# Optimization experiments

Measured on AMD Instinct MI355X. Metric: run time of the kernel, lower is better.

## Reference

```python
import jax, jax.numpy as jnp
import numpy as np

B, F, T, EPT, S, E, H, LVL = 16384, 512, 4, 2, 2, 256, 128, 2

def _ple_level(xs_task, x_sh, w_task, b_task, w_sh, b_sh, w_gate, b_gate, w_gsh=None, b_gsh=None):
    # xs_task: [T,B,I] per-task inputs; x_sh: [B,I] shared input
    task_out = jax.nn.relu(jnp.einsum('tbi,teio->tbeo', xs_task, w_task) + b_task[:, None])  # [T,B,EPT,E]
    sh_out = jax.nn.relu(jnp.einsum('bi,sio->bso', x_sh, w_sh) + b_sh)                       # [B,S,E]
    t = task_out.shape[0]
    experts = jnp.concatenate([task_out, jnp.broadcast_to(sh_out[None], (t,) + sh_out.shape)], axis=2)  # [T,B,EPT+S,E]
    gate = jax.nn.softmax(jnp.einsum('tbi,tig->tbg', xs_task, w_gate) + b_gate[:, None], axis=-1)
    task_next = jnp.einsum('tbg,tbge->tbe', gate, experts)  # [T,B,E]
    sh_next = None
    if w_gsh is not None:
        # all experts ordered task0_exp0, task0_exp1, task1_exp0, ..., then shared
        bsz = x_sh.shape[0]
        all_exp = jnp.concatenate([jnp.transpose(task_out, (1, 0, 2, 3)).reshape(bsz, -1, task_out.shape[-1]), sh_out], axis=1)
        gsh = jax.nn.softmax(x_sh @ w_gsh + b_gsh, axis=-1)
        sh_next = jnp.einsum('bg,bge->be', gsh, all_exp)
    return task_next, sh_next

def setup_inputs() -> dict:
    key = jax.random.key(0)
    ks = jax.random.split(key, 16)
    sc = 0.02
    d = {
        'x': jax.random.normal(ks[0], (B, F), jnp.float32),
        # level 0 (in_dim=F, has shared gate)
        'w_task0': jax.random.normal(ks[1], (T, EPT, F, E), jnp.float32) * sc,
        'b_task0': jnp.zeros((T, EPT, E), jnp.float32),
        'w_sh0': jax.random.normal(ks[2], (S, F, E), jnp.float32) * sc,
        'b_sh0': jnp.zeros((S, E), jnp.float32),
        'w_gate0': jax.random.normal(ks[3], (T, F, EPT + S), jnp.float32) * sc,
        'b_gate0': jnp.zeros((T, EPT + S), jnp.float32),
        'w_gsh0': jax.random.normal(ks[4], (F, T * EPT + S), jnp.float32) * sc,
        'b_gsh0': jnp.zeros((T * EPT + S,), jnp.float32),
        # level 1 (last; in_dim=E, no shared gate)
        'w_task1': jax.random.normal(ks[5], (T, EPT, E, E), jnp.float32) * sc,
        'b_task1': jnp.zeros((T, EPT, E), jnp.float32),
        'w_sh1': jax.random.normal(ks[6], (S, E, E), jnp.float32) * sc,
        'b_sh1': jnp.zeros((S, E), jnp.float32),
        'w_gate1': jax.random.normal(ks[7], (T, E, EPT + S), jnp.float32) * sc,
        'b_gate1': jnp.zeros((T, EPT + S), jnp.float32),
        # towers
        'w_tw': jax.random.normal(ks[8], (T, E, H), jnp.float32) * sc,
        'b_tw': jnp.zeros((T, H), jnp.float32),
        'w_out': jax.random.normal(ks[9], (T, H, 2), jnp.float32) * sc,
        'b_out': jnp.zeros((T, 2), jnp.float32),
    }
    return d

def reference(x, w_task0, b_task0, w_sh0, b_sh0, w_gate0, b_gate0, w_gsh0, b_gsh0,
              w_task1, b_task1, w_sh1, b_sh1, w_gate1, b_gate1,
              w_tw, b_tw, w_out, b_out):
    xs_task = jnp.broadcast_to(x[None], (T,) + x.shape)  # all tasks see same input at level 0
    t1, sh1 = _ple_level(xs_task, x, w_task0, b_task0, w_sh0, b_sh0, w_gate0, b_gate0, w_gsh0, b_gsh0)
    t2, _ = _ple_level(t1, sh1, w_task1, b_task1, w_sh1, b_sh1, w_gate1, b_gate1)
    h = jax.nn.relu(jnp.einsum('tbe,teh->tbh', t2, w_tw) + b_tw[:, None])
    logits = jnp.einsum('tbh,tho->tbo', h, w_out) + b_out[:, None]
    p = jax.nn.softmax(logits, axis=-1)
    return jnp.clip(p, 1e-15, 1.0 - 1e-15)  # [T,B,2]
```

## Files before the change

### kernel.cpp

```cpp
#include <hip/hip_runtime.h>

typedef unsigned short u16;
typedef __bf16 bf16x8 __attribute__((ext_vector_type(8)));
typedef float f32x4 __attribute__((ext_vector_type(4)));
typedef u16 u16x8 __attribute__((ext_vector_type(8)));

#define B_ 16384

__device__ __forceinline__ u16 f2b(float f){
  unsigned u = __builtin_bit_cast(unsigned, f);
  u = (u + 0x7FFFu + ((u >> 16) & 1u)) >> 16;
  return (u16)u;
}
__device__ __forceinline__ float b2f(u16 v){
  return __builtin_bit_cast(float, ((unsigned)v) << 16);
}
__device__ __forceinline__ void ld8(const u16* __restrict__ p, float* f){
  u16x8 v = *(const u16x8*)p;
  #pragma unroll
  for (int j = 0; j < 8; ++j) f[j] = b2f(v[j]);
}
__device__ __forceinline__ void st8(u16* __restrict__ p, const float* f){
  u16x8 v;
  #pragma unroll
  for (int j = 0; j < 8; ++j) v[j] = f2b(f[j]);
  *(u16x8*)p = v;
}

__device__ __forceinline__ void gload16(const u16* g, u16* lds){
  __builtin_amdgcn_global_load_lds(
      (const __attribute__((address_space(1))) unsigned int*)g,
      (__attribute__((address_space(3))) unsigned int*)lds, 16, 0, 0);
}

__device__ __forceinline__ void core32(const u16* __restrict__ A,
                                       const u16* __restrict__ Wt,
                                       int K, int m0, int n0, int nt,
                                       u16* sm, f32x4 acc[4][4])
{
  const int tid = threadIdx.x, lane = tid & 63, wave = tid >> 6;
  const int wm = ((tid >> 7) & 3) * 64;
  const int wn = ((tid >> 6) & 1) * 64;

  #pragma unroll
  for (int m = 0; m < 4; ++m)
    #pragma unroll
    for (int n = 0; n < 4; ++n) acc[m][n] = (f32x4){0.f, 0.f, 0.f, 0.f};

  const int s_    = (lane & 7) ^ ((lane >> 3) & 7);
  const int srow2 = 2 * (lane >> 3) + (s_ >> 2);
  const int sk    = (s_ & 3) * 8;
  const u16* gsrc[3];
  int gdst[3];
  #pragma unroll
  for (int i = 0; i < 3; ++i) {
    int c = wave * 3 + i;
    if (c < 16) {
      gsrc[i] = A + (size_t)(m0 + c * 16 + srow2) * K + sk;
      gdst[i] = c * 512;
    } else {
      gsrc[i] = Wt + (size_t)(n0 + (c - 16) * 16 + srow2) * K + sk;
      gdst[i] = 8192 + (c - 16) * 512;
    }
  }

  int aoff[4], boff[4];
  #pragma unroll
  for (int m = 0; m < 4; ++m) {
    int r = wm + m * 16 + (lane & 15);
    int L = r >> 1;
    int phys = (((r & 1) << 2) + (lane >> 4)) ^ (L & 7);
    aoff[m] = L * 64 + phys * 8;
  }
  #pragma unroll
  for (int n = 0; n < 4; ++n) {
    int r = wn + n * 16 + (lane & 15);
    int L = r >> 1;
    int phys = (((r & 1) << 2) + (lane >> 4)) ^ (L & 7);
    boff[n] = 8192 + L * 64 + phys * 8;
  }

  #pragma unroll
  for (int j = 0; j < 2; ++j) {
    u16* sl = sm + j * 12288;
    #pragma unroll
    for (int i = 0; i < 3; ++i) gload16(gsrc[i] + j * 32, sl + gdst[i]);
  }
  asm volatile("s_waitcnt vmcnt(3)" ::: "memory");
  __builtin_amdgcn_s_barrier();

  int cs = 0;
  for (int j = 0; j < nt; ++j) {
    if (j + 2 < nt) {
      int ns = cs + 2; ns = (ns >= 3) ? ns - 3 : ns;
      u16* sl = sm + ns * 12288;
      #pragma unroll
      for (int i = 0; i < 3; ++i) gload16(gsrc[i] + (size_t)(j + 2) * 32, sl + gdst[i]);
    }
    const u16* sa = sm + cs * 12288;
    bf16x8 av[4], bv[4];
    #pragma unroll
    for (int m = 0; m < 4; ++m) av[m] = *(const bf16x8*)(sa + aoff[m]);
    #pragma unroll
    for (int n = 0; n < 4; ++n) bv[n] = *(const bf16x8*)(sa + boff[n]);
    __builtin_amdgcn_s_setprio(1);
    #pragma unroll
    for (int m = 0; m < 4; ++m)
      #pragma unroll
      for (int n = 0; n < 4; ++n)
        acc[m][n] = __builtin_amdgcn_mfma_f32_16x16x32_bf16(av[m], bv[n], acc[m][n], 0, 0, 0);
    __builtin_amdgcn_s_setprio(0);
    if (j + 2 < nt)      asm volatile("s_waitcnt vmcnt(3)" ::: "memory");
    else if (j + 1 < nt) asm volatile("s_waitcnt vmcnt(0)" ::: "memory");
    __builtin_amdgcn_s_barrier();
    cs = (cs == 2) ? 0 : cs + 1;
  }
}


__global__ __launch_bounds__(512) void k_gemm0(const u16* __restrict__ xb,
    const u16* __restrict__ Wt0, const float* __restrict__ bias0,
    u16* __restrict__ E0, float* __restrict__ G0L)
{
  __shared__ __align__(16) u16 sm[36864];
  f32x4 acc[4][4];
  const int bid = blockIdx.x;
  const int swz = (bid & 7) * 168 + (bid >> 3);
  const int m0 = (swz / 21) * 256, n0 = (swz % 21) * 128;
  core32(xb, Wt0, 512, m0, n0, 16, sm, acc);
  const int lane = threadIdx.x & 63;
  const int wm = ((threadIdx.x >> 7) & 3) * 64, wn = ((threadIdx.x >> 6) & 1) * 64;
  #pragma unroll
  for (int mi = 0; mi < 4; ++mi)
    #pragma unroll
    for (int ni = 0; ni < 4; ++ni) {
      int gcol = n0 + wn + ni * 16 + (lane & 15);
      float bias = bias0[gcol];
      #pragma unroll
      for (int q = 0; q < 4; ++q) {
        int grow = m0 + wm + mi * 16 + ((lane >> 4) << 2) + q;
        float v = acc[mi][ni][q] + bias;
        if (gcol < 2560)      E0[(size_t)grow * 2560 + gcol] = f2b(fmaxf(v, 0.f));
        else if (gcol < 2586) G0L[(size_t)grow * 26 + (gcol - 2560)] = v;
      }
    }
}

__global__ __launch_bounds__(256) void k_mix0(const u16* __restrict__ E0,
    const float* __restrict__ G0L, const float* __restrict__ WG1T,
    const float* __restrict__ b_gate1, u16* __restrict__ T1SH,
    float* __restrict__ G1S)
{
  const int b = blockIdx.x * 8 + (threadIdx.x >> 5);
  const int e0 = (threadIdx.x & 31) * 8;
  const float* gl = G0L + (size_t)b * 26;
  float g[4][4];
  #pragma unroll
  for (int t = 0; t < 4; ++t) {
    float l0 = gl[t*4+0], l1 = gl[t*4+1], l2 = gl[t*4+2], l3 = gl[t*4+3];
    float m = fmaxf(fmaxf(l0, l1), fmaxf(l2, l3));
    float e0e = expf(l0-m), e1 = expf(l1-m), e2 = expf(l2-m), e3 = expf(l3-m);
    float inv = 1.f / (e0e + e1 + e2 + e3);
    g[t][0] = e0e*inv; g[t][1] = e1*inv; g[t][2] = e2*inv; g[t][3] = e3*inv;
  }
  float gs[10];
  {
    float m = gl[16];
    #pragma unroll
    for (int j = 1; j < 10; ++j) m = fmaxf(m, gl[16 + j]);
    float s = 0.f;
    #pragma unroll
    for (int j = 0; j < 10; ++j) { gs[j] = expf(gl[16 + j] - m); s += gs[j]; }
    float inv = 1.f / s;
    #pragma unroll
    for (int j = 0; j < 10; ++j) gs[j] *= inv;
  }
  const u16* row = E0 + (size_t)b * 2560;
  float sh0[8], sh1[8], shacc[8];
  ld8(row + 2048 + e0, sh0);
  ld8(row + 2304 + e0, sh1);
  #pragma unroll
  for (int j = 0; j < 8; ++j) shacc[j] = gs[8]*sh0[j] + gs[9]*sh1[j];
  float gp[16];
  #pragma unroll
  for (int t = 0; t < 4; ++t) {
    float te0[8], te1[8], v[8];
    ld8(row + (t*2+0)*256 + e0, te0);
    ld8(row + (t*2+1)*256 + e0, te1);
    #pragma unroll
    for (int j = 0; j < 8; ++j) {
      v[j] = g[t][0]*te0[j] + g[t][1]*te1[j] + g[t][2]*sh0[j] + g[t][3]*sh1[j];
      shacc[j] += gs[t*2+0]*te0[j] + gs[t*2+1]*te1[j];
    }
    st8(T1SH + ((size_t)t * B_ + b) * 256 + e0, v);
    #pragma unroll
    for (int gg = 0; gg < 4; ++gg) {
      const float* wv = WG1T + ((size_t)(t * 4 + gg) * 256 + e0);
      float s = 0.f;
      #pragma unroll
      for (int j = 0; j < 8; ++j) s += v[j] * wv[j];
      gp[t * 4 + gg] = s;
    }
  }
  st8(T1SH + ((size_t)4 * B_ + b) * 256 + e0, shacc);
  #pragma unroll
  for (int i = 0; i < 16; ++i) {
    #pragma unroll
    for (int off = 1; off < 32; off <<= 1)
      gp[i] += __shfl_xor(gp[i], off, 32);
  }
  if ((threadIdx.x & 31) == 0) {
    float* orow = G1S + (size_t)b * 16;
    #pragma unroll
    for (int z = 0; z < 4; ++z) {
      float l0 = gp[z*4+0] + b_gate1[z*4+0];
      float l1 = gp[z*4+1] + b_gate1[z*4+1];
      float l2 = gp[z*4+2] + b_gate1[z*4+2];
      float l3 = gp[z*4+3] + b_gate1[z*4+3];
      float m = fmaxf(fmaxf(l0, l1), fmaxf(l2, l3));
      float x0 = expf(l0-m), x1 = expf(l1-m), x2 = expf(l2-m), x3 = expf(l3-m);
      float inv = 1.f / (x0 + x1 + x2 + x3);
      orow[z*4+0] = x0*inv; orow[z*4+1] = x1*inv;
      orow[z*4+2] = x2*inv; orow[z*4+3] = x3*inv;
    }
  }
}

__global__ __launch_bounds__(512) void k_gemm1(const u16* __restrict__ T1SH,
    const u16* __restrict__ Wt1, const float* __restrict__ bias1,
    u16* __restrict__ E1, u16* __restrict__ SH1E)
{
  __shared__ __align__(16) u16 sm[36864];
  f32x4 acc[4][4];
  const int bid = blockIdx.x;
  const int swz = (bid & 7) * 160 + (bid >> 3);
  const int mi_ = swz / 20, pan = swz % 20;
  const int z  = pan >> 2;
  const int n0 = (pan & 3) * 128;
  const int m0 = mi_ * 256;
  core32(T1SH + (size_t)z * B_ * 256, Wt1 + (size_t)z * 512 * 256, 256, m0, n0, 8, sm, acc);
  const int lane = threadIdx.x & 63;
  const int wm = ((threadIdx.x >> 7) & 3) * 64, wn = ((threadIdx.x >> 6) & 1) * 64;
  const float* bias = bias1 + z * 512;
  #pragma unroll
  for (int mi = 0; mi < 4; ++mi)
    #pragma unroll
    for (int ni = 0; ni < 4; ++ni) {
      int gcol = n0 + wn + ni * 16 + (lane & 15);
      float bv = bias[gcol];
      #pragma unroll
      for (int q = 0; q < 4; ++q) {
        int grow = m0 + wm + mi * 16 + ((lane >> 4) << 2) + q;
        float v = fmaxf(acc[mi][ni][q] + bv, 0.f);
        if (z < 4) E1[((size_t)z * B_ + grow) * 512 + gcol] = f2b(v);
        else       SH1E[(size_t)grow * 512 + gcol] = f2b(v);
      }
    }
}

__global__ __launch_bounds__(256) void k_mix1(const u16* __restrict__ E1,
    const float* __restrict__ G1S, const u16* __restrict__ SH1E, u16* __restrict__ T2)
{
  const int b = blockIdx.x * 8 + (threadIdx.x >> 5);
  const int e0 = (threadIdx.x & 31) * 8;
  float sh0[8], sh1[8];
  ld8(SH1E + (size_t)b * 512 + e0, sh0);
  ld8(SH1E + (size_t)b * 512 + 256 + e0, sh1);
  const float* gr = G1S + (size_t)b * 16;
  #pragma unroll
  for (int t = 0; t < 4; ++t) {
    float g0 = gr[t*4+0], g1 = gr[t*4+1], g2 = gr[t*4+2], g3 = gr[t*4+3];
    float te0[8], te1[8], v[8];
    ld8(E1 + ((size_t)t * B_ + b) * 512 + e0, te0);
    ld8(E1 + ((size_t)t * B_ + b) * 512 + 256 + e0, te1);
    #pragma unroll
    for (int j = 0; j < 8; ++j)
      v[j] = g0*te0[j] + g1*te1[j] + g2*sh0[j] + g3*sh1[j];
    st8(T2 + ((size_t)t * B_ + b) * 256 + e0, v);
  }
}

__device__ __forceinline__ void gemm_core4(const u16* __restrict__ A,
                                           const u16* __restrict__ Wt,
                                           int K, int m0, int n0, int nt,
                                           u16* sm, f32x4 acc[4][4])
{
  const int tid  = threadIdx.x;
  const int lane = tid & 63;
  const int wave = tid >> 6;
  const int wm   = ((tid >> 7) & 1) * 64;
  const int wn   = ((tid >> 6) & 1) * 64;

  f32x4 zero = {0.f, 0.f, 0.f, 0.f};
  #pragma unroll
  for (int mi = 0; mi < 4; ++mi)
    #pragma unroll
    for (int ni = 0; ni < 4; ++ni) acc[mi][ni] = zero;

  const int srow  = lane >> 3;
  const int gslot = (lane & 7) ^ srow;
  const u16* gsrc[8];
  int gdst[8];
  #pragma unroll
  for (int i = 0; i < 8; ++i) {
    int c = wave * 8 + i;
    if (c < 16) {
      gsrc[i] = A + (size_t)(m0 + c * 8 + srow) * K + gslot * 8;
      gdst[i] = c * 512;
    } else {
      gsrc[i] = Wt + (size_t)(n0 + (c - 16) * 8 + srow) * K + gslot * 8;
      gdst[i] = 8192 + (c - 16) * 512;
    }
  }

  int aoff[2][4], boff[2][4];
  #pragma unroll
  for (int kk = 0; kk < 2; ++kk) {
    #pragma unroll
    for (int m = 0; m < 4; ++m) {
      int r = wm + m * 16 + (lane & 15);
      aoff[kk][m] = r * 64 + (((kk * 4 + (lane >> 4)) ^ (r & 7)) * 8);
    }
    #pragma unroll
    for (int n = 0; n < 4; ++n) {
      int r = wn + n * 16 + (lane & 15);
      boff[kk][n] = 8192 + r * 64 + (((kk * 4 + (lane >> 4)) ^ (r & 7)) * 8);
    }
  }

  #pragma unroll
  for (int i = 0; i < 8; ++i) gload16(gsrc[i], sm + gdst[i]);
  asm volatile("s_waitcnt vmcnt(0)" ::: "memory");
  __builtin_amdgcn_s_barrier();

  for (int j = 0; j < nt; ++j) {
    if (j + 1 < nt) {
      u16* base = sm + ((j + 1) & 1) * 16384;
      #pragma unroll
      for (int i = 0; i < 8; ++i) gload16(gsrc[i] + (size_t)(j + 1) * 64, base + gdst[i]);
    }
    const u16* sa = sm + (j & 1) * 16384;
    #pragma unroll
    for (int kk = 0; kk < 2; ++kk) {
      bf16x8 av[4], bv[4];
      #pragma unroll
      for (int m = 0; m < 4; ++m) av[m] = *(const bf16x8*)(sa + aoff[kk][m]);
      #pragma unroll
      for (int n = 0; n < 4; ++n) bv[n] = *(const bf16x8*)(sa + boff[kk][n]);
      #pragma unroll
      for (int m = 0; m < 4; ++m)
        #pragma unroll
        for (int n = 0; n < 4; ++n)
          acc[m][n] = __builtin_amdgcn_mfma_f32_16x16x32_bf16(av[m], bv[n], acc[m][n], 0, 0, 0);
    }
    if (j + 1 < nt) {
      asm volatile("s_waitcnt vmcnt(0)" ::: "memory");
      __builtin_amdgcn_s_barrier();
    }
  }
}

__global__ __launch_bounds__(256) void k_tower(const u16* __restrict__ T2,
    const u16* __restrict__ Wtw, const float* __restrict__ b_tw,
    const float* __restrict__ w_out, const float* __restrict__ b_out,
    float* __restrict__ out)
{
  __shared__ __align__(16) u16 sm[32768];
  __shared__ float part[2][128][2];
  f32x4 acc[4][4];
  const int z = blockIdx.z;
  const int m0 = blockIdx.x * 128;
  gemm_core4(T2 + (size_t)z * B_ * 256, Wtw + (size_t)z * 128 * 256, 256, m0, 0, 4, sm, acc);
  const int lane = threadIdx.x & 63;
  const int wm = ((threadIdx.x >> 7) & 1) * 64, wn = ((threadIdx.x >> 6) & 1) * 64;
  #pragma unroll
  for (int mi = 0; mi < 4; ++mi) {
    #pragma unroll
    for (int r = 0; r < 4; ++r) {
      float p0 = 0.f, p1 = 0.f;
      #pragma unroll
      for (int ni = 0; ni < 4; ++ni) {
        int col = wn + ni * 16 + (lane & 15);
        float h = fmaxf(acc[mi][ni][r] + b_tw[z * 128 + col], 0.f);
        p0 += h * w_out[(z * 128 + col) * 2 + 0];
        p1 += h * w_out[(z * 128 + col) * 2 + 1];
      }
      #pragma unroll
      for (int off = 1; off < 16; off <<= 1) {
        p0 += __shfl_xor(p0, off);
        p1 += __shfl_xor(p1, off);
      }
      if ((lane & 15) == 0) {
        int rowl = wm + mi * 16 + ((lane >> 4) << 2) + r;
        part[wn >> 6][rowl][0] = p0;
        part[wn >> 6][rowl][1] = p1;
      }
    }
  }
  __syncthreads();
  if (threadIdx.x < 128) {
    int rowl = threadIdx.x;
    float l0 = part[0][rowl][0] + part[1][rowl][0] + b_out[z * 2 + 0];
    float l1 = part[0][rowl][1] + part[1][rowl][1] + b_out[z * 2 + 1];
    float mx = fmaxf(l0, l1);
    float e0 = expf(l0 - mx), e1 = expf(l1 - mx);
    float inv = 1.f / (e0 + e1);
    float p0 = fminf(fmaxf(e0 * inv, 1e-15f), 1.0f);
    float p1 = fminf(fmaxf(e1 * inv, 1e-15f), 1.0f);
    size_t o = ((size_t)z * B_ + m0 + rowl) * 2;
    out[o] = p0; out[o + 1] = p1;
  }
}

__global__ void k_prep(const float* __restrict__ x,
    const float* __restrict__ w_task0, const float* __restrict__ b_task0,
    const float* __restrict__ w_sh0,   const float* __restrict__ b_sh0,
    const float* __restrict__ w_gate0, const float* __restrict__ b_gate0,
    const float* __restrict__ w_gsh0,  const float* __restrict__ b_gsh0,
    const float* __restrict__ w_task1, const float* __restrict__ b_task1,
    const float* __restrict__ w_sh1,   const float* __restrict__ b_sh1,
    const float* __restrict__ w_gate1, const float* __restrict__ w_tw,
    u16* __restrict__ xb, u16* __restrict__ Wt0, float* __restrict__ bias0,
    u16* __restrict__ Wt1, float* __restrict__ bias1, u16* __restrict__ Wtw,
    float* __restrict__ WG1T)
{
  size_t i = (size_t)blockIdx.x * 256 + threadIdx.x;
  const size_t S_X8  = (size_t)16384 * 512 / 8;
  const size_t S_WT0 = (size_t)2816 * 512;
  const size_t S_B0  = 2816;
  const size_t S_WT1 = (size_t)5 * 512 * 256;
  const size_t S_B1  = 5 * 512;
  const size_t S_WTW = (size_t)4 * 128 * 256;
  const size_t S_WG1 = 4096;

  if (i < S_X8) {
    size_t o = i * 8;
    float4 a = *(const float4*)(x + o);
    float4 b = *(const float4*)(x + o + 4);
    u16x8 v;
    v[0] = f2b(a.x); v[1] = f2b(a.y); v[2] = f2b(a.z); v[3] = f2b(a.w);
    v[4] = f2b(b.x); v[5] = f2b(b.y); v[6] = f2b(b.z); v[7] = f2b(b.w);
    *(u16x8*)(xb + o) = v;
    return;
  }
  i -= S_X8;
  if (i < S_WT0) {
    int c = (int)(i / 512), f = (int)(i % 512);
    float v = 0.f;
    if (c < 2048)      { int te = c >> 8, o = c & 255; v = w_task0[((size_t)te * 512 + f) * 256 + o]; }
    else if (c < 2560) { int s = (c - 2048) >> 8, o = c & 255; v = w_sh0[((size_t)s * 512 + f) * 256 + o]; }
    else if (c < 2576) { int q = c - 2560; int t = q >> 2, gg = q & 3; v = w_gate0[((size_t)t * 512 + f) * 4 + gg]; }
    else if (c < 2586) { int j = c - 2576; v = w_gsh0[(size_t)f * 10 + j]; }
    Wt0[i] = f2b(v);
    return;
  }
  i -= S_WT0;
  if (i < S_B0) {
    int c = (int)i; float v = 0.f;
    if (c < 2048)      { int te = c >> 8, o = c & 255; v = b_task0[te * 256 + o]; }
    else if (c < 2560) { int s = (c - 2048) >> 8, o = c & 255; v = b_sh0[s * 256 + o]; }
    else if (c < 2576) { v = b_gate0[c - 2560]; }
    else if (c < 2586) { v = b_gsh0[c - 2576]; }
    bias0[c] = v;
    return;
  }
  i -= S_B0;
  if (i < S_WT1) {
    int z = (int)(i / (512 * 256)); int rem = (int)(i % (512 * 256));
    int c = rem / 256, f = rem % 256;
    float v;
    if (z < 4) { int ee = c >> 8, o = c & 255; v = w_task1[(((size_t)(z * 2 + ee)) * 256 + f) * 256 + o]; }
    else       { int s = c >> 8, o = c & 255; v = w_sh1[((size_t)s * 256 + f) * 256 + o]; }
    Wt1[i] = f2b(v);
    return;
  }
  i -= S_WT1;
  if (i < S_B1) {
    int z = (int)(i / 512); int c = (int)(i % 512);
    float v;
    if (z < 4) { int ee = c >> 8, o = c & 255; v = b_task1[(z * 2 + ee) * 256 + o]; }
    else       { int s = c >> 8, o = c & 255; v = b_sh1[s * 256 + o]; }
    bias1[(size_t)z * 512 + c] = v;
    return;
  }
  i -= S_B1;
  if (i < S_WTW) {
    int z = (int)(i / (128 * 256)); int rem = (int)(i % (128 * 256));
    int h = rem / 256, f = rem % 256;
    Wtw[i] = f2b(w_tw[((size_t)z * 256 + f) * 128 + h]);
    return;
  }
  i -= S_WTW;
  if (i < S_WG1) {
    int t = (int)(i >> 10), gg = (int)((i >> 8) & 3), e = (int)(i & 255);
    WG1T[i] = w_gate1[((size_t)t * 256 + e) * 4 + gg];
    return;
  }
}

extern "C" void kernel_launch(void* const* d_in, const int* in_sizes, int n_in,
                              void* d_out, int out_size, void* d_ws, size_t ws_size,
                              hipStream_t stream)
{
  (void)in_sizes; (void)n_in; (void)out_size; (void)ws_size;
  const float* x       = (const float*)d_in[0];
  const float* w_task0 = (const float*)d_in[1];
  const float* b_task0 = (const float*)d_in[2];
  const float* w_sh0   = (const float*)d_in[3];
  const float* b_sh0   = (const float*)d_in[4];
  const float* w_gate0 = (const float*)d_in[5];
  const float* b_gate0 = (const float*)d_in[6];
  const float* w_gsh0  = (const float*)d_in[7];
  const float* b_gsh0  = (const float*)d_in[8];
  const float* w_task1 = (const float*)d_in[9];
  const float* b_task1 = (const float*)d_in[10];
  const float* w_sh1   = (const float*)d_in[11];
  const float* b_sh1   = (const float*)d_in[12];
  const float* w_gate1 = (const float*)d_in[13];
  const float* b_gate1 = (const float*)d_in[14];
  const float* w_tw    = (const float*)d_in[15];
  const float* b_tw    = (const float*)d_in[16];
  const float* w_out   = (const float*)d_in[17];
  const float* b_out   = (const float*)d_in[18];
  float* out = (float*)d_out;

  char* ws = (char*)d_ws;
  u16*   XB    = (u16*)  (ws + 0);
  u16*   SH1E  = (u16*)  (ws + 0);
  u16*   WT0   = (u16*)  (ws + 16777216);
  float* BIAS0 = (float*)(ws + 19660800);
  u16*   WT1   = (u16*)  (ws + 19672064);
  float* BIAS1 = (float*)(ws + 20982784);
  u16*   WTW   = (u16*)  (ws + 20993024);
  u16*   E0    = (u16*)  (ws + 21255168);
  u16*   T2    = (u16*)  (ws + 21255168);
  float* G0L   = (float*)(ws + 105141248);
  u16*   T1SH  = (u16*)  (ws + 106845184);
  u16*   E1    = (u16*)  (ws + 148788224);
  float* G1S   = (float*)(ws + 215897088);
  float* WG1T  = (float*)(ws + 216945664);

  k_prep<<<12837, 256, 0, stream>>>(x, w_task0, b_task0, w_sh0, b_sh0, w_gate0, b_gate0,
      w_gsh0, b_gsh0, w_task1, b_task1, w_sh1, b_sh1, w_gate1, w_tw,
      XB, WT0, BIAS0, WT1, BIAS1, WTW, WG1T);
  k_gemm0<<<1344, 512, 0, stream>>>(XB, WT0, BIAS0, E0, G0L);
  k_mix0<<<2048, 256, 0, stream>>>(E0, G0L, WG1T, b_gate1, T1SH, G1S);
  k_gemm1<<<1280, 512, 0, stream>>>(T1SH, WT1, BIAS1, E1, SH1E);
  k_mix1<<<2048, 256, 0, stream>>>(E1, G1S, SH1E, T2);
  k_tower<<<dim3(128, 1, 4), 256, 0, stream>>>(T2, WTW, b_tw, w_out, b_out, out);
}
```

Baseline: 179.1 us.

## Fuse level-1 gate mixing into tower GEMM A-tile staging

```diff
diff --git a/kernel.cpp b/kernel.cpp
--- a/kernel.cpp
+++ b/kernel.cpp
@@ -258,109 +258,8 @@
     }
 }
 
-__global__ __launch_bounds__(256) void k_mix1(const u16* __restrict__ E1,
-    const float* __restrict__ G1S, const u16* __restrict__ SH1E, u16* __restrict__ T2)
-{
-  const int b = blockIdx.x * 8 + (threadIdx.x >> 5);
-  const int e0 = (threadIdx.x & 31) * 8;
-  float sh0[8], sh1[8];
-  ld8(SH1E + (size_t)b * 512 + e0, sh0);
-  ld8(SH1E + (size_t)b * 512 + 256 + e0, sh1);
-  const float* gr = G1S + (size_t)b * 16;
-  #pragma unroll
-  for (int t = 0; t < 4; ++t) {
-    float g0 = gr[t*4+0], g1 = gr[t*4+1], g2 = gr[t*4+2], g3 = gr[t*4+3];
-    float te0[8], te1[8], v[8];
-    ld8(E1 + ((size_t)t * B_ + b) * 512 + e0, te0);
-    ld8(E1 + ((size_t)t * B_ + b) * 512 + 256 + e0, te1);
-    #pragma unroll
-    for (int j = 0; j < 8; ++j)
-      v[j] = g0*te0[j] + g1*te1[j] + g2*sh0[j] + g3*sh1[j];
-    st8(T2 + ((size_t)t * B_ + b) * 256 + e0, v);
-  }
-}
-
-__device__ __forceinline__ void gemm_core4(const u16* __restrict__ A,
-                                           const u16* __restrict__ Wt,
-                                           int K, int m0, int n0, int nt,
-                                           u16* sm, f32x4 acc[4][4])
-{
-  const int tid  = threadIdx.x;
-  const int lane = tid & 63;
-  const int wave = tid >> 6;
-  const int wm   = ((tid >> 7) & 1) * 64;
-  const int wn   = ((tid >> 6) & 1) * 64;
-
-  f32x4 zero = {0.f, 0.f, 0.f, 0.f};
-  #pragma unroll
-  for (int mi = 0; mi < 4; ++mi)
-    #pragma unroll
-    for (int ni = 0; ni < 4; ++ni) acc[mi][ni] = zero;
-
-  const int srow  = lane >> 3;
-  const int gslot = (lane & 7) ^ srow;
-  const u16* gsrc[8];
-  int gdst[8];
-  #pragma unroll
-  for (int i = 0; i < 8; ++i) {
-    int c = wave * 8 + i;
-    if (c < 16) {
-      gsrc[i] = A + (size_t)(m0 + c * 8 + srow) * K + gslot * 8;
-      gdst[i] = c * 512;
-    } else {
-      gsrc[i] = Wt + (size_t)(n0 + (c - 16) * 8 + srow) * K + gslot * 8;
-      gdst[i] = 8192 + (c - 16) * 512;
-    }
-  }
-
-  int aoff[2][4], boff[2][4];
-  #pragma unroll
-  for (int kk = 0; kk < 2; ++kk) {
-    #pragma unroll
-    for (int m = 0; m < 4; ++m) {
-      int r = wm + m * 16 + (lane & 15);
-      aoff[kk][m] = r * 64 + (((kk * 4 + (lane >> 4)) ^ (r & 7)) * 8);
-    }
-    #pragma unroll
-    for (int n = 0; n < 4; ++n) {
-      int r = wn + n * 16 + (lane & 15);
-      boff[kk][n] = 8192 + r * 64 + (((kk * 4 + (lane >> 4)) ^ (r & 7)) * 8);
-    }
-  }
-
-  #pragma unroll
-  for (int i = 0; i < 8; ++i) gload16(gsrc[i], sm + gdst[i]);
-  asm volatile("s_waitcnt vmcnt(0)" ::: "memory");
-  __builtin_amdgcn_s_barrier();
-
-  for (int j = 0; j < nt; ++j) {
-    if (j + 1 < nt) {
-      u16* base = sm + ((j + 1) & 1) * 16384;
-      #pragma unroll
-      for (int i = 0; i < 8; ++i) gload16(gsrc[i] + (size_t)(j + 1) * 64, base + gdst[i]);
-    }
-    const u16* sa = sm + (j & 1) * 16384;
-    #pragma unroll
-    for (int kk = 0; kk < 2; ++kk) {
-      bf16x8 av[4], bv[4];
-      #pragma unroll
-      for (int m = 0; m < 4; ++m) av[m] = *(const bf16x8*)(sa + aoff[kk][m]);
-      #pragma unroll
-      for (int n = 0; n < 4; ++n) bv[n] = *(const bf16x8*)(sa + boff[kk][n]);
-      #pragma unroll
-      for (int m = 0; m < 4; ++m)
-        #pragma unroll
-        for (int n = 0; n < 4; ++n)
-          acc[m][n] = __builtin_amdgcn_mfma_f32_16x16x32_bf16(av[m], bv[n], acc[m][n], 0, 0, 0);
-    }
-    if (j + 1 < nt) {
-      asm volatile("s_waitcnt vmcnt(0)" ::: "memory");
-      __builtin_amdgcn_s_barrier();
-    }
-  }
-}
-
-__global__ __launch_bounds__(256) void k_tower(const u16* __restrict__ T2,
+__global__ __launch_bounds__(256) void k_tower2(const u16* __restrict__ E1,
+    const u16* __restrict__ SH1E, const float* __restrict__ G1S,
     const u16* __restrict__ Wtw, const float* __restrict__ b_tw,
     const float* __restrict__ w_out, const float* __restrict__ b_out,
     float* __restrict__ out)
@@ -370,9 +269,89 @@
   f32x4 acc[4][4];
   const int z = blockIdx.z;
   const int m0 = blockIdx.x * 128;
-  gemm_core4(T2 + (size_t)z * B_ * 256, Wtw + (size_t)z * 128 * 256, 256, m0, 0, 4, sm, acc);
-  const int lane = threadIdx.x & 63;
-  const int wm = ((threadIdx.x >> 7) & 1) * 64, wn = ((threadIdx.x >> 6) & 1) * 64;
+  const int tid = threadIdx.x, lane = tid & 63, wave = tid >> 6;
+  const int wm = ((tid >> 7) & 1) * 64, wn = ((tid >> 6) & 1) * 64;
+
+  #pragma unroll
+  for (int mi = 0; mi < 4; ++mi)
+    #pragma unroll
+    for (int ni = 0; ni < 4; ++ni) acc[mi][ni] = (f32x4){0.f, 0.f, 0.f, 0.f};
+
+  const int srow  = lane >> 3;
+  const int gslot = (lane & 7) ^ srow;
+  const int koff0 = gslot * 8;
+
+  int growA[4], adst[4], bdst[4];
+  const u16* bsrc[4];
+  #pragma unroll
+  for (int i = 0; i < 4; ++i) {
+    int c = wave * 4 + i;
+    growA[i] = m0 + c * 8 + srow;
+    adst[i]  = c * 512;
+    bsrc[i]  = Wtw + (size_t)z * 128 * 256 + (size_t)(c * 8 + srow) * 256 + koff0;
+    bdst[i]  = 8192 + c * 512;
+  }
+  const u16* E1z = E1 + (size_t)z * B_ * 512;
+
+  int aoff[2][4], boff[2][4];
+  #pragma unroll
+  for (int kk = 0; kk < 2; ++kk) {
+    #pragma unroll
+    for (int m = 0; m < 4; ++m) {
+      int r = wm + m * 16 + (lane & 15);
+      aoff[kk][m] = r * 64 + (((kk * 4 + (lane >> 4)) ^ (r & 7)) * 8);
+    }
+    #pragma unroll
+    for (int n = 0; n < 4; ++n) {
+      int r = wn + n * 16 + (lane & 15);
+      boff[kk][n] = 8192 + r * 64 + (((kk * 4 + (lane >> 4)) ^ (r & 7)) * 8);
+    }
+  }
+
+  #define STAGE_T(J, BUF) do {                                                 \
+    u16* buf_ = (BUF);                                                         \
+    _Pragma("unroll")                                                          \
+    for (int i_ = 0; i_ < 4; ++i_) {                                           \
+      size_t eoff_ = (size_t)growA[i_] * 512 + (J) * 64 + koff0;               \
+      u16x8 ea_ = *(const u16x8*)(E1z + eoff_);                                \
+      u16x8 eb_ = *(const u16x8*)(E1z + eoff_ + 256);                          \
+      u16x8 sa_ = *(const u16x8*)(SH1E + eoff_);                               \
+      u16x8 sb_ = *(const u16x8*)(SH1E + eoff_ + 256);                         \
+      float4 g_ = *(const float4*)(G1S + (size_t)growA[i_] * 16 + z * 4);      \
+      u16x8 o_;                                                                \
+      _Pragma("unroll")                                                        \
+      for (int jj_ = 0; jj_ < 8; ++jj_)                                        \
+        o_[jj_] = f2b(g_.x * b2f(ea_[jj_]) + g_.y * b2f(eb_[jj_])              \
+                    + g_.z * b2f(sa_[jj_]) + g_.w * b2f(sb_[jj_]));            \
+      *(uint4*)(buf_ + adst[i_] + lane * 8) = __builtin_bit_cast(uint4, o_);   \
+      gload16(bsrc[i_] + (J) * 64, buf_ + bdst[i_]);                           \
+    }                                                                          \
+  } while (0)
+
+  STAGE_T(0, sm);
+  __syncthreads();
+
+  #pragma unroll
+  for (int t = 0; t < 4; ++t) {
+    if (t + 1 < 4) STAGE_T(t + 1, sm + ((t + 1) & 1) * 16384);
+    const u16* sa = sm + (t & 1) * 16384;
+    #pragma unroll
+    for (int kk = 0; kk < 2; ++kk) {
+      bf16x8 av[4], bv[4];
+      #pragma unroll
+      for (int m = 0; m < 4; ++m) av[m] = *(const bf16x8*)(sa + aoff[kk][m]);
+      #pragma unroll
+      for (int n = 0; n < 4; ++n) bv[n] = *(const bf16x8*)(sa + boff[kk][n]);
+      #pragma unroll
+      for (int m = 0; m < 4; ++m)
+        #pragma unroll
+        for (int n = 0; n < 4; ++n)
+          acc[m][n] = __builtin_amdgcn_mfma_f32_16x16x32_bf16(av[m], bv[n], acc[m][n], 0, 0, 0);
+    }
+    if (t + 1 < 4) __syncthreads();
+  }
+  #undef STAGE_T
+
   #pragma unroll
   for (int mi = 0; mi < 4; ++mi) {
     #pragma unroll
@@ -533,7 +512,6 @@
   float* BIAS1 = (float*)(ws + 20982784);
   u16*   WTW   = (u16*)  (ws + 20993024);
   u16*   E0    = (u16*)  (ws + 21255168);
-  u16*   T2    = (u16*)  (ws + 21255168);
   float* G0L   = (float*)(ws + 105141248);
   u16*   T1SH  = (u16*)  (ws + 106845184);
   u16*   E1    = (u16*)  (ws + 148788224);
@@ -546,6 +524,5 @@
   k_gemm0<<<1344, 512, 0, stream>>>(XB, WT0, BIAS0, E0, G0L);
   k_mix0<<<2048, 256, 0, stream>>>(E0, G0L, WG1T, b_gate1, T1SH, G1S);
   k_gemm1<<<1280, 512, 0, stream>>>(T1SH, WT1, BIAS1, E1, SH1E);
-  k_mix1<<<2048, 256, 0, stream>>>(E1, G1S, SH1E, T2);
-  k_tower<<<dim3(128, 1, 4), 256, 0, stream>>>(T2, WTW, b_tw, w_out, b_out, out);
-}
+  k_tower2<<<dim3(128, 1, 4), 256, 0, stream>>>(E1, SH1E, G1S, WTW, b_tw, w_out, b_out, out);
+}
```

After: 172.0 us, median of 2. 1.04x faster.
